# Optimization experiments

Measured on AMD Instinct MI355X. Metric: run time of the kernel, lower is better.

Reference implementation:

```python
import jax, jax.numpy as jnp
import numpy as np

KE = 14.3996454784255
P = 6  # polynomial cutoff order
A_EXP = 0.3
A_PREFACTOR = 0.4543
C = jnp.array([0.1818, 0.5099, 0.2802, 0.02817], dtype=jnp.float32)
K = jnp.array([3.2, 0.9423, 0.4028, 0.2016], dtype=jnp.float32)

N_NODES = 100000
N_EDGES = 6400000
N_ELEM = 10
N_RADII = 119


def setup_inputs() -> dict:
    key = jax.random.key(0)
    k1, k2, k3, k4, k5 = jax.random.split(key, 5)
    # edge distances in a physically plausible range (avoid x ~ 0 -> 1/x blowup)
    x = jax.random.uniform(k1, (N_EDGES, 1), dtype=jnp.float32) * 4.0 + 0.05
    node_attrs = jax.random.uniform(k2, (N_NODES, N_ELEM), dtype=jnp.float32)
    edge_index = jax.random.randint(k3, (2, N_EDGES), 0, N_NODES, dtype=jnp.int64)
    atomic_numbers = jax.random.randint(k4, (N_ELEM,), 1, N_RADII, dtype=jnp.int64)
    # covalent radii table (stand-in for ase.data.covalent_radii), ~0.3..2.6 Angstrom
    covalent_radii = 0.3 + 2.3 * jax.random.uniform(k5, (N_RADII,), dtype=jnp.float32)
    return {
        "x": x,
        "node_attrs": node_attrs,
        "edge_index": edge_index,
        "atomic_numbers": atomic_numbers,
        "covalent_radii": covalent_radii,
    }


def _envelope(x, r_max, p):
    r = x / r_max
    env = (1.0
           - (p + 1.0) * (p + 2.0) / 2.0 * r ** p
           + p * (p + 2.0) * r ** (p + 1)
           - p * (p + 1.0) / 2.0 * r ** (p + 2))
    return env * (x < r_max)


def reference(x, node_attrs, edge_index, atomic_numbers, covalent_radii):
    sender = edge_index[0]    # [E]
    receiver = edge_index[1]  # [E]
    # per-node atomic number from one-hot-ish node_attrs
    node_Z = atomic_numbers[jnp.argmax(node_attrs, axis=1)][:, None]  # [N,1] int
    Z_u = node_Z[sender]   # [E,1] int
    Z_v = node_Z[receiver] # [E,1] int
    Zu_f = Z_u.astype(x.dtype)
    Zv_f = Z_v.astype(x.dtype)
    a = A_PREFACTOR * 0.529 / (Zu_f ** A_EXP + Zv_f ** A_EXP)  # [E,1]
    r_over_a = x / a
    phi = (C[0] * jnp.exp(-K[0] * r_over_a)
           + C[1] * jnp.exp(-K[1] * r_over_a)
           + C[2] * jnp.exp(-K[2] * r_over_a)
           + C[3] * jnp.exp(-K[3] * r_over_a))
    v_edges = KE * Zu_f * Zv_f / x * phi  # [E,1]
    r_max = covalent_radii[Z_u[:, 0]][:, None] + covalent_radii[Z_v[:, 0]][:, None]  # [E,1]
    env = _envelope(x, r_max, float(P))
    v_edges = 0.5 * v_edges * env
    V_ZBL = jax.ops.segment_sum(v_edges, receiver, num_segments=node_attrs.shape[0])  # [N,1]
    return V_ZBL[:, 0]
```

## Files before the change

kernel.cpp:

```cpp
#include <hip/hip_runtime.h>

#define KE_CONST 14.3996454784255f

#define P2_SHIFT 15
#define P2_CHUNK 32768
#define SCAN_B2  64
#define SCAN_THR 1024
#define MAXC     4
#define MAXE     16

__global__ void zbl_prep_elem(const float* __restrict__ node_attrs,
                              unsigned char* __restrict__ elem,
                              int n_nodes, int n_elem) {
    int n = blockIdx.x * blockDim.x + threadIdx.x;
    if (n >= n_nodes) return;
    const float* row = node_attrs + (size_t)n * n_elem;
    float best = row[0];
    int bi = 0;
    for (int i = 1; i < n_elem; ++i) {
        float v = row[i];
        if (v > best) { best = v; bi = i; }
    }
    elem[n] = (unsigned char)bi;
}

__global__ void zbl_prep_pairs(const int* __restrict__ atomic_numbers,
                               const float* __restrict__ covalent_radii,
                               float4* __restrict__ pair_tab,
                               int n_elem) {
    int t = threadIdx.x;
    int np = n_elem * n_elem;
    if (t >= np) return;
    int eu = t / n_elem;
    int ev = t - eu * n_elem;
    int Zu = atomic_numbers[eu];
    int Zv = atomic_numbers[ev];
    float zu = (float)Zu, zv = (float)Zv;
    float inv_a = (__powf(zu, 0.3f) + __powf(zv, 0.3f)) * (1.0f / (0.4543f * 0.529f));
    float kezz  = 0.5f * KE_CONST * zu * zv;
    float rmax  = covalent_radii[Zu] + covalent_radii[Zv];
    pair_tab[t] = make_float4(inv_a, kezz, rmax, 1.0f / rmax);
}

__device__ __forceinline__ unsigned enc_val_p(float xv, const float4& pt) {
    float t = xv * pt.x;
    float phi = 0.1818f  * __expf(-3.2f    * t)
              + 0.5099f  * __expf(-0.9423f * t)
              + 0.2802f  * __expf(-0.4028f * t)
              + 0.02817f * __expf(-0.2016f * t);
    float rr = xv * pt.w;
    float r2 = rr * rr;
    float r6 = r2 * r2 * r2;
    float env = 1.0f - 28.0f * r6 + 48.0f * r6 * rr - 21.0f * r6 * r2;
    float val = fmaxf(pt.y * phi / xv * env, 0.0f);
    unsigned e = (__float_as_uint(val) + 0x8000u) >> 16;
    if (e > 0x7FFFu) e = 0x7FFFu;
    return (xv < pt.z) ? e : 0u;
}

__global__ __launch_bounds__(256)
void zbl_dense(const float* __restrict__ x,
               const int* __restrict__ ei,
               const unsigned char* __restrict__ elem,
               const float4* __restrict__ pair_tab,
               unsigned* __restrict__ packed,
               int n_edges, int n_elem) {
    __shared__ float4 pt[MAXE * MAXE];
    int np = n_elem * n_elem;
    for (int i = threadIdx.x; i < np; i += 256) pt[i] = pair_tab[i];
    __syncthreads();

    int t = blockIdx.x * blockDim.x + threadIdx.x;
    int base = t * 4;
    if (base + 4 <= n_edges) {
        int4   s4 = *(const int4*)(ei + base);
        int4   r4 = *(const int4*)(ei + n_edges + base);
        float4 x4 = *(const float4*)(x + base);
        unsigned es0 = elem[s4.x], es1 = elem[s4.y], es2 = elem[s4.z], es3 = elem[s4.w];
        unsigned er0 = elem[r4.x], er1 = elem[r4.y], er2 = elem[r4.z], er3 = elem[r4.w];
        float4 p0 = pt[es0 * n_elem + er0];
        float4 p1 = pt[es1 * n_elem + er1];
        float4 p2 = pt[es2 * n_elem + er2];
        float4 p3 = pt[es3 * n_elem + er3];
        uint4 o;
        o.x = ((unsigned)r4.x << 15) | enc_val_p(x4.x, p0);
        o.y = ((unsigned)r4.y << 15) | enc_val_p(x4.y, p1);
        o.z = ((unsigned)r4.z << 15) | enc_val_p(x4.z, p2);
        o.w = ((unsigned)r4.w << 15) | enc_val_p(x4.w, p3);
        *(uint4*)(packed + base) = o;
    } else {
        for (int e = base; e < n_edges; ++e) {
            unsigned es = elem[ei[e]];
            unsigned er = elem[ei[n_edges + e]];
            int r = ei[n_edges + e];
            packed[e] = ((unsigned)r << 15) | enc_val_p(x[e], pt[es * n_elem + er]);
        }
    }
}

__global__ __launch_bounds__(SCAN_THR)
void zbl_scan(const unsigned* __restrict__ packed,
              float* __restrict__ partial,
              int n_edges) {
    unsigned c = blockIdx.x >> 6;
    int      j = blockIdx.x & (SCAN_B2 - 1);

    __shared__ __align__(16) float acc[P2_CHUNK];
    for (int i = threadIdx.x * 4; i < P2_CHUNK; i += SCAN_THR * 4)
        *(float4*)&acc[i] = make_float4(0.f, 0.f, 0.f, 0.f);
    __syncthreads();

    long long e0 = (((long long)j * n_edges) / SCAN_B2) & ~3LL;
    long long e1 = (j == SCAN_B2 - 1) ? (long long)n_edges
                                      : ((((long long)(j + 1) * n_edges) / SCAN_B2) & ~3LL);
    long long vend = e1 & ~3LL;

    for (long long b = e0 + (long long)threadIdx.x * 4; b + 4 <= vend;
         b += (long long)SCAN_THR * 4) {
        uint4 p = *(const uint4*)(packed + b);
        if ((p.x >> 30) == c) atomicAdd(&acc[(p.x >> 15) & (P2_CHUNK - 1)],
                                        __uint_as_float((p.x & 0x7FFFu) << 16));
        if ((p.y >> 30) == c) atomicAdd(&acc[(p.y >> 15) & (P2_CHUNK - 1)],
                                        __uint_as_float((p.y & 0x7FFFu) << 16));
        if ((p.z >> 30) == c) atomicAdd(&acc[(p.z >> 15) & (P2_CHUNK - 1)],
                                        __uint_as_float((p.z & 0x7FFFu) << 16));
        if ((p.w >> 30) == c) atomicAdd(&acc[(p.w >> 15) & (P2_CHUNK - 1)],
                                        __uint_as_float((p.w & 0x7FFFu) << 16));
    }
    for (long long e = vend + threadIdx.x; e < e1; e += SCAN_THR) {
        unsigned w = packed[e];
        if ((w >> 30) == c) atomicAdd(&acc[(w >> 15) & (P2_CHUNK - 1)],
                                      __uint_as_float((w & 0x7FFFu) << 16));
    }

    __syncthreads();
    float* pp = partial + (size_t)blockIdx.x * P2_CHUNK;
    for (int i = threadIdx.x * 4; i < P2_CHUNK; i += SCAN_THR * 4)
        *(float4*)(pp + i) = *(const float4*)&acc[i];
}

__global__ void zbl_reduce(const float* __restrict__ partial,
                           float* __restrict__ out,
                           int n_nodes) {
    int i = blockIdx.x * blockDim.x + threadIdx.x;
    if (i >= n_nodes) return;
    int c  = i >> P2_SHIFT;
    int li = i & (P2_CHUNK - 1);
    const float* p = partial + ((size_t)c * SCAN_B2) * P2_CHUNK + li;
    float s0 = 0.f, s1 = 0.f, s2 = 0.f, s3 = 0.f;
    #pragma unroll
    for (int j = 0; j < SCAN_B2; j += 4) {
        s0 += p[(size_t)(j + 0) * P2_CHUNK];
        s1 += p[(size_t)(j + 1) * P2_CHUNK];
        s2 += p[(size_t)(j + 2) * P2_CHUNK];
        s3 += p[(size_t)(j + 3) * P2_CHUNK];
    }
    out[i] = (s0 + s1) + (s2 + s3);
}

__global__ void zbl_node_prep(const float* __restrict__ node_attrs,
                              const int* __restrict__ atomic_numbers,
                              const float* __restrict__ covalent_radii,
                              float4* __restrict__ node_data,
                              float* __restrict__ out_zero,
                              int n_nodes, int n_elem) {
    int n = blockIdx.x * blockDim.x + threadIdx.x;
    if (n >= n_nodes) return;
    const float* row = node_attrs + (size_t)n * n_elem;
    float best = row[0];
    int bi = 0;
    for (int i = 1; i < n_elem; ++i) {
        float v = row[i];
        if (v > best) { best = v; bi = i; }
    }
    int Z = atomic_numbers[bi];
    float zf = (float)Z;
    node_data[n] = make_float4(zf, __powf(zf, 0.3f), covalent_radii[Z], 0.0f);
    out_zero[n] = 0.0f;
}

__global__ void zbl_edge_atomic(const float* __restrict__ x,
                                const int* __restrict__ edge_index,
                                const float4* __restrict__ node_data,
                                float* __restrict__ out,
                                int n_edges) {
    int e = blockIdx.x * blockDim.x + threadIdx.x;
    if (e >= n_edges) return;
    int snd = edge_index[e];
    int r = edge_index[n_edges + e];
    float xv = x[e];
    float4 du = node_data[snd];
    float4 dv = node_data[r];
    float rmax = du.z + dv.z;
    if (xv >= rmax) return;
    const float inv_a_pref = 1.0f / (0.4543f * 0.529f);
    float t = xv * (du.y + dv.y) * inv_a_pref;
    float phi = 0.1818f  * __expf(-3.2f    * t)
              + 0.5099f  * __expf(-0.9423f * t)
              + 0.2802f  * __expf(-0.4028f * t)
              + 0.02817f * __expf(-0.2016f * t);
    float v = KE_CONST * du.x * dv.x * phi / xv;
    float rr = xv / rmax;
    float r2 = rr * rr;
    float r6 = r2 * r2 * r2;
    float env = 1.0f - 28.0f * r6 + 48.0f * r6 * rr - 21.0f * r6 * r2;
    atomicAdd(&out[r], 0.5f * v * env);
}

extern "C" void kernel_launch(void* const* d_in, const int* in_sizes, int n_in,
                              void* d_out, int out_size, void* d_ws, size_t ws_size,
                              hipStream_t stream) {
    const float* x              = (const float*)d_in[0];
    const float* node_attrs     = (const float*)d_in[1];
    const int*   edge_index     = (const int*)d_in[2];
    const int*   atomic_numbers = (const int*)d_in[3];
    const float* covalent_radii = (const float*)d_in[4];
    float* out = (float*)d_out;

    int n_edges = in_sizes[0];
    int n_elem  = in_sizes[3];
    int n_nodes = in_sizes[1] / n_elem;

    int C = (n_nodes + P2_CHUNK - 1) >> P2_SHIFT;
    size_t elem_bytes   = (((size_t)n_nodes) + 255) & ~(size_t)255;
    size_t pair_bytes   = ((size_t)MAXE * MAXE * sizeof(float4) + 255) & ~(size_t)255;
    size_t packed_bytes = (((size_t)n_edges * sizeof(unsigned)) + 255) & ~(size_t)255;
    size_t part_bytes   = (size_t)C * SCAN_B2 * P2_CHUNK * sizeof(float);
    bool fast = (C >= 1) && (C <= MAXC) && (n_nodes <= (1 << 17)) &&
                (n_elem >= 1) && (n_elem <= MAXE) && ((n_edges & 3) == 0) &&
                (ws_size >= elem_bytes + pair_bytes + packed_bytes + part_bytes);

    if (fast) {
        unsigned char* elem     = (unsigned char*)d_ws;
        float4*        pair_tab = (float4*)((char*)d_ws + elem_bytes);
        unsigned*      packed   = (unsigned*)((char*)d_ws + elem_bytes + pair_bytes);
        float*         part     = (float*)((char*)d_ws + elem_bytes + pair_bytes + packed_bytes);

        zbl_prep_elem<<<(n_nodes + 255) / 256, 256, 0, stream>>>(
            node_attrs, elem, n_nodes, n_elem);
        zbl_prep_pairs<<<1, 256, 0, stream>>>(
            atomic_numbers, covalent_radii, pair_tab, n_elem);

        zbl_dense<<<(n_edges / 4 + 255) / 256, 256, 0, stream>>>(
            x, edge_index, elem, pair_tab, packed, n_edges, n_elem);

        zbl_scan<<<C * SCAN_B2, SCAN_THR, 0, stream>>>(packed, part, n_edges);

        zbl_reduce<<<(n_nodes + 255) / 256, 256, 0, stream>>>(part, out, n_nodes);
        return;
    }

    float4* node_data = (float4*)d_ws;
    zbl_node_prep<<<(n_nodes + 255) / 256, 256, 0, stream>>>(
        node_attrs, atomic_numbers, covalent_radii, node_data,
        out, n_nodes, n_elem);
    zbl_edge_atomic<<<(n_edges + 255) / 256, 256, 0, stream>>>(
        x, edge_index, node_data, out, n_edges);
}
```

Before: 202.5 us.

## Fuse edge evaluation into chunked shared-memory scatter, dropping packed buffer

The separate dense pass that wrote packed receiver/bf16-value words is removed. Each scatter block now reads x, sender and receiver directly, computes the ZBL edge value in full fp32 and atomically adds it into its LDS chunk. This avoids writing and re-reading a 25.6 MB intermediate and one kernel launch. In exchange, every edge is recomputed once per node chunk (4 chunks), and the raw edge_index and x loads are read by each chunk instead of once.

```diff
diff --git a/kernel.cpp b/kernel.cpp
--- a/kernel.cpp
+++ b/kernel.cpp
@@ -42,95 +42,73 @@
     pair_tab[t] = make_float4(inv_a, kezz, rmax, 1.0f / rmax);
 }
 
-__device__ __forceinline__ unsigned enc_val_p(float xv, const float4& pt) {
-    float t = xv * pt.x;
+__device__ __forceinline__ float edge_val(float xv, const float4& p) {
+    float t = xv * p.x;
     float phi = 0.1818f  * __expf(-3.2f    * t)
               + 0.5099f  * __expf(-0.9423f * t)
               + 0.2802f  * __expf(-0.4028f * t)
               + 0.02817f * __expf(-0.2016f * t);
-    float rr = xv * pt.w;
+    float rr = xv * p.w;
     float r2 = rr * rr;
     float r6 = r2 * r2 * r2;
     float env = 1.0f - 28.0f * r6 + 48.0f * r6 * rr - 21.0f * r6 * r2;
-    float val = fmaxf(pt.y * phi / xv * env, 0.0f);
-    unsigned e = (__float_as_uint(val) + 0x8000u) >> 16;
-    if (e > 0x7FFFu) e = 0x7FFFu;
-    return (xv < pt.z) ? e : 0u;
-}
-
-__global__ __launch_bounds__(256)
-void zbl_dense(const float* __restrict__ x,
+    return p.y * phi / xv * env;
+}
+
+__global__ __launch_bounds__(SCAN_THR)
+void zbl_fused(const float* __restrict__ x,
                const int* __restrict__ ei,
                const unsigned char* __restrict__ elem,
                const float4* __restrict__ pair_tab,
-               unsigned* __restrict__ packed,
+               float* __restrict__ partial,
                int n_edges, int n_elem) {
+    unsigned c = blockIdx.x >> 6;
+    int      j = blockIdx.x & (SCAN_B2 - 1);
+
+    __shared__ __align__(16) float acc[P2_CHUNK];
     __shared__ float4 pt[MAXE * MAXE];
     int np = n_elem * n_elem;
-    for (int i = threadIdx.x; i < np; i += 256) pt[i] = pair_tab[i];
+    for (int i = threadIdx.x; i < np; i += SCAN_THR) pt[i] = pair_tab[i];
+    for (int i = threadIdx.x * 4; i < P2_CHUNK; i += SCAN_THR * 4)
+        *(float4*)&acc[i] = make_float4(0.f, 0.f, 0.f, 0.f);
     __syncthreads();
 
-    int t = blockIdx.x * blockDim.x + threadIdx.x;
-    int base = t * 4;
-    if (base + 4 <= n_edges) {
-        int4   s4 = *(const int4*)(ei + base);
-        int4   r4 = *(const int4*)(ei + n_edges + base);
-        float4 x4 = *(const float4*)(x + base);
+    const int* __restrict__ rcv = ei + n_edges;
+    long long e0 = (((long long)j * n_edges) / SCAN_B2) & ~3LL;
+    long long e1 = (j == SCAN_B2 - 1) ? (long long)n_edges
+                                      : ((((long long)(j + 1) * n_edges) / SCAN_B2) & ~3LL);
+    long long vend = e1 & ~3LL;
+
+    for (long long b = e0 + (long long)threadIdx.x * 4; b + 4 <= vend;
+         b += (long long)SCAN_THR * 4) {
+        int4   r4 = *(const int4*)(rcv + b);
+        int4   s4 = *(const int4*)(ei + b);
+        float4 x4 = *(const float4*)(x + b);
         unsigned es0 = elem[s4.x], es1 = elem[s4.y], es2 = elem[s4.z], es3 = elem[s4.w];
         unsigned er0 = elem[r4.x], er1 = elem[r4.y], er2 = elem[r4.z], er3 = elem[r4.w];
         float4 p0 = pt[es0 * n_elem + er0];
         float4 p1 = pt[es1 * n_elem + er1];
         float4 p2 = pt[es2 * n_elem + er2];
         float4 p3 = pt[es3 * n_elem + er3];
-        uint4 o;
-        o.x = ((unsigned)r4.x << 15) | enc_val_p(x4.x, p0);
-        o.y = ((unsigned)r4.y << 15) | enc_val_p(x4.y, p1);
-        o.z = ((unsigned)r4.z << 15) | enc_val_p(x4.z, p2);
-        o.w = ((unsigned)r4.w << 15) | enc_val_p(x4.w, p3);
-        *(uint4*)(packed + base) = o;
-    } else {
-        for (int e = base; e < n_edges; ++e) {
-            unsigned es = elem[ei[e]];
-            unsigned er = elem[ei[n_edges + e]];
-            int r = ei[n_edges + e];
-            packed[e] = ((unsigned)r << 15) | enc_val_p(x[e], pt[es * n_elem + er]);
-        }
-    }
-}
-
-__global__ __launch_bounds__(SCAN_THR)
-void zbl_scan(const unsigned* __restrict__ packed,
-              float* __restrict__ partial,
-              int n_edges) {
-    unsigned c = blockIdx.x >> 6;
-    int      j = blockIdx.x & (SCAN_B2 - 1);
-
-    __shared__ __align__(16) float acc[P2_CHUNK];
-    for (int i = threadIdx.x * 4; i < P2_CHUNK; i += SCAN_THR * 4)
-        *(float4*)&acc[i] = make_float4(0.f, 0.f, 0.f, 0.f);
-    __syncthreads();
-
-    long long e0 = (((long long)j * n_edges) / SCAN_B2) & ~3LL;
-    long long e1 = (j == SCAN_B2 - 1) ? (long long)n_edges
-                                      : ((((long long)(j + 1) * n_edges) / SCAN_B2) & ~3LL);
-    long long vend = e1 & ~3LL;
-
-    for (long long b = e0 + (long long)threadIdx.x * 4; b + 4 <= vend;
-         b += (long long)SCAN_THR * 4) {
-        uint4 p = *(const uint4*)(packed + b);
-        if ((p.x >> 30) == c) atomicAdd(&acc[(p.x >> 15) & (P2_CHUNK - 1)],
-                                        __uint_as_float((p.x & 0x7FFFu) << 16));
-        if ((p.y >> 30) == c) atomicAdd(&acc[(p.y >> 15) & (P2_CHUNK - 1)],
-                                        __uint_as_float((p.y & 0x7FFFu) << 16));
-        if ((p.z >> 30) == c) atomicAdd(&acc[(p.z >> 15) & (P2_CHUNK - 1)],
-                                        __uint_as_float((p.z & 0x7FFFu) << 16));
-        if ((p.w >> 30) == c) atomicAdd(&acc[(p.w >> 15) & (P2_CHUNK - 1)],
-                                        __uint_as_float((p.w & 0x7FFFu) << 16));
+        float v0 = edge_val(x4.x, p0);
+        float v1 = edge_val(x4.y, p1);
+        float v2 = edge_val(x4.z, p2);
+        float v3 = edge_val(x4.w, p3);
+        if (((unsigned)(r4.x >> P2_SHIFT) == c) & (x4.x < p0.z))
+            atomicAdd(&acc[r4.x & (P2_CHUNK - 1)], v0);
+        if (((unsigned)(r4.y >> P2_SHIFT) == c) & (x4.y < p1.z))
+            atomicAdd(&acc[r4.y & (P2_CHUNK - 1)], v1);
+        if (((unsigned)(r4.z >> P2_SHIFT) == c) & (x4.z < p2.z))
+            atomicAdd(&acc[r4.z & (P2_CHUNK - 1)], v2);
+        if (((unsigned)(r4.w >> P2_SHIFT) == c) & (x4.w < p3.z))
+            atomicAdd(&acc[r4.w & (P2_CHUNK - 1)], v3);
     }
     for (long long e = vend + threadIdx.x; e < e1; e += SCAN_THR) {
-        unsigned w = packed[e];
-        if ((w >> 30) == c) atomicAdd(&acc[(w >> 15) & (P2_CHUNK - 1)],
-                                      __uint_as_float((w & 0x7FFFu) << 16));
+        int r = rcv[e];
+        if ((unsigned)(r >> P2_SHIFT) != c) continue;
+        float4 p = pt[elem[ei[e]] * n_elem + elem[r]];
+        float xv = x[e];
+        if (xv < p.z) atomicAdd(&acc[r & (P2_CHUNK - 1)], edge_val(xv, p));
     }
 
     __syncthreads();
@@ -222,29 +200,25 @@
     int n_nodes = in_sizes[1] / n_elem;
 
     int C = (n_nodes + P2_CHUNK - 1) >> P2_SHIFT;
-    size_t elem_bytes   = (((size_t)n_nodes) + 255) & ~(size_t)255;
-    size_t pair_bytes   = ((size_t)MAXE * MAXE * sizeof(float4) + 255) & ~(size_t)255;
-    size_t packed_bytes = (((size_t)n_edges * sizeof(unsigned)) + 255) & ~(size_t)255;
-    size_t part_bytes   = (size_t)C * SCAN_B2 * P2_CHUNK * sizeof(float);
+    size_t elem_bytes = (((size_t)n_nodes) + 255) & ~(size_t)255;
+    size_t pair_bytes = ((size_t)MAXE * MAXE * sizeof(float4) + 255) & ~(size_t)255;
+    size_t part_bytes = (size_t)C * SCAN_B2 * P2_CHUNK * sizeof(float);
     bool fast = (C >= 1) && (C <= MAXC) && (n_nodes <= (1 << 17)) &&
-                (n_elem >= 1) && (n_elem <= MAXE) && ((n_edges & 3) == 0) &&
-                (ws_size >= elem_bytes + pair_bytes + packed_bytes + part_bytes);
+                (n_elem >= 1) && (n_elem <= MAXE) &&
+                (ws_size >= elem_bytes + pair_bytes + part_bytes);
 
     if (fast) {
         unsigned char* elem     = (unsigned char*)d_ws;
         float4*        pair_tab = (float4*)((char*)d_ws + elem_bytes);
-        unsigned*      packed   = (unsigned*)((char*)d_ws + elem_bytes + pair_bytes);
-        float*         part     = (float*)((char*)d_ws + elem_bytes + pair_bytes + packed_bytes);
+        float*         part     = (float*)((char*)d_ws + elem_bytes + pair_bytes);
 
         zbl_prep_elem<<<(n_nodes + 255) / 256, 256, 0, stream>>>(
             node_attrs, elem, n_nodes, n_elem);
         zbl_prep_pairs<<<1, 256, 0, stream>>>(
             atomic_numbers, covalent_radii, pair_tab, n_elem);
 
-        zbl_dense<<<(n_edges / 4 + 255) / 256, 256, 0, stream>>>(
-            x, edge_index, elem, pair_tab, packed, n_edges, n_elem);
-
-        zbl_scan<<<C * SCAN_B2, SCAN_THR, 0, stream>>>(packed, part, n_edges);
+        zbl_fused<<<C * SCAN_B2, SCAN_THR, 0, stream>>>(
+            x, edge_index, elem, pair_tab, part, n_edges, n_elem);
 
         zbl_reduce<<<(n_nodes + 255) / 256, 256, 0, stream>>>(part, out, n_nodes);
         return;
```

Result: slower. 268.3 us (+32.5%).

## Stage node element table in LDS for dense edge pass with persistent blocks

Applied to the files above, without the earlier changes.

The dense edge kernel now copies the whole per-node element byte table (up to 128 KB) into shared memory in each block. The per-edge sender and receiver element lookups then hit LDS instead of issuing random global byte gathers. To pay for that copy, the kernel switches to 256 persistent blocks of 1024 threads, each striding over a contiguous edge range, with a scalar tail loop that also drops the old requirement that the edge count be a multiple of four. The cost is repeated table loads per block and only one block per CU because of the large LDS footprint.

```diff
diff --git a/kernel.cpp b/kernel.cpp
--- a/kernel.cpp
+++ b/kernel.cpp
@@ -8,6 +8,9 @@
 #define SCAN_THR 1024
 #define MAXC     4
 #define MAXE     16
+#define ELEM_CAP 131072
+#define DN_THR   1024
+#define DN_BLOCKS 256
 
 __global__ void zbl_prep_elem(const float* __restrict__ node_attrs,
                               unsigned char* __restrict__ elem,
@@ -42,40 +45,51 @@
     pair_tab[t] = make_float4(inv_a, kezz, rmax, 1.0f / rmax);
 }
 
-__device__ __forceinline__ unsigned enc_val_p(float xv, const float4& pt) {
-    float t = xv * pt.x;
+__device__ __forceinline__ unsigned enc_val_p(float xv, const float4& p) {
+    float t = xv * p.x;
     float phi = 0.1818f  * __expf(-3.2f    * t)
               + 0.5099f  * __expf(-0.9423f * t)
               + 0.2802f  * __expf(-0.4028f * t)
               + 0.02817f * __expf(-0.2016f * t);
-    float rr = xv * pt.w;
+    float rr = xv * p.w;
     float r2 = rr * rr;
     float r6 = r2 * r2 * r2;
     float env = 1.0f - 28.0f * r6 + 48.0f * r6 * rr - 21.0f * r6 * r2;
-    float val = fmaxf(pt.y * phi / xv * env, 0.0f);
+    float val = fmaxf(p.y * phi / xv * env, 0.0f);
     unsigned e = (__float_as_uint(val) + 0x8000u) >> 16;
     if (e > 0x7FFFu) e = 0x7FFFu;
-    return (xv < pt.z) ? e : 0u;
-}
-
-__global__ __launch_bounds__(256)
-void zbl_dense(const float* __restrict__ x,
-               const int* __restrict__ ei,
-               const unsigned char* __restrict__ elem,
-               const float4* __restrict__ pair_tab,
-               unsigned* __restrict__ packed,
-               int n_edges, int n_elem) {
+    return (xv < p.z) ? e : 0u;
+}
+
+__global__ __launch_bounds__(DN_THR)
+void zbl_dense_lds(const float* __restrict__ x,
+                   const int* __restrict__ ei,
+                   const unsigned char* __restrict__ elem_g,
+                   const float4* __restrict__ pair_tab,
+                   unsigned* __restrict__ packed,
+                   int n_edges, int n_elem, int n_nodes) {
+    __shared__ __align__(16) unsigned char elem[ELEM_CAP];
     __shared__ float4 pt[MAXE * MAXE];
+
     int np = n_elem * n_elem;
-    for (int i = threadIdx.x; i < np; i += 256) pt[i] = pair_tab[i];
+    for (int i = threadIdx.x; i < np; i += DN_THR) pt[i] = pair_tab[i];
+    int nwords = (n_nodes + 15) >> 4;
+    const uint4* eg4 = (const uint4*)elem_g;
+    uint4* el4 = (uint4*)elem;
+    for (int i = threadIdx.x; i < nwords; i += DN_THR) el4[i] = eg4[i];
     __syncthreads();
 
-    int t = blockIdx.x * blockDim.x + threadIdx.x;
-    int base = t * 4;
-    if (base + 4 <= n_edges) {
-        int4   s4 = *(const int4*)(ei + base);
-        int4   r4 = *(const int4*)(ei + n_edges + base);
-        float4 x4 = *(const float4*)(x + base);
+    long long e0 = (((long long)blockIdx.x * n_edges) / DN_BLOCKS) & ~3LL;
+    long long e1 = (blockIdx.x == DN_BLOCKS - 1)
+                     ? (long long)n_edges
+                     : ((((long long)(blockIdx.x + 1) * n_edges) / DN_BLOCKS) & ~3LL);
+    long long vend = e1 & ~3LL;
+
+    for (long long b = e0 + (long long)threadIdx.x * 4; b + 4 <= vend;
+         b += (long long)DN_THR * 4) {
+        int4   s4 = *(const int4*)(ei + b);
+        int4   r4 = *(const int4*)(ei + n_edges + b);
+        float4 x4 = *(const float4*)(x + b);
         unsigned es0 = elem[s4.x], es1 = elem[s4.y], es2 = elem[s4.z], es3 = elem[s4.w];
         unsigned er0 = elem[r4.x], er1 = elem[r4.y], er2 = elem[r4.z], er3 = elem[r4.w];
         float4 p0 = pt[es0 * n_elem + er0];
@@ -87,14 +101,12 @@
         o.y = ((unsigned)r4.y << 15) | enc_val_p(x4.y, p1);
         o.z = ((unsigned)r4.z << 15) | enc_val_p(x4.z, p2);
         o.w = ((unsigned)r4.w << 15) | enc_val_p(x4.w, p3);
-        *(uint4*)(packed + base) = o;
-    } else {
-        for (int e = base; e < n_edges; ++e) {
-            unsigned es = elem[ei[e]];
-            unsigned er = elem[ei[n_edges + e]];
-            int r = ei[n_edges + e];
-            packed[e] = ((unsigned)r << 15) | enc_val_p(x[e], pt[es * n_elem + er]);
-        }
+        *(uint4*)(packed + b) = o;
+    }
+    for (long long e = vend + threadIdx.x; e < e1; e += DN_THR) {
+        int r = ei[n_edges + e];
+        float4 p = pt[elem[ei[e]] * n_elem + elem[r]];
+        packed[e] = ((unsigned)r << 15) | enc_val_p(x[e], p);
     }
 }
 
@@ -226,8 +238,8 @@
     size_t pair_bytes   = ((size_t)MAXE * MAXE * sizeof(float4) + 255) & ~(size_t)255;
     size_t packed_bytes = (((size_t)n_edges * sizeof(unsigned)) + 255) & ~(size_t)255;
     size_t part_bytes   = (size_t)C * SCAN_B2 * P2_CHUNK * sizeof(float);
-    bool fast = (C >= 1) && (C <= MAXC) && (n_nodes <= (1 << 17)) &&
-                (n_elem >= 1) && (n_elem <= MAXE) && ((n_edges & 3) == 0) &&
+    bool fast = (C >= 1) && (C <= MAXC) && (n_nodes <= ELEM_CAP) &&
+                (n_elem >= 1) && (n_elem <= MAXE) &&
                 (ws_size >= elem_bytes + pair_bytes + packed_bytes + part_bytes);
 
     if (fast) {
@@ -241,8 +253,8 @@
         zbl_prep_pairs<<<1, 256, 0, stream>>>(
             atomic_numbers, covalent_radii, pair_tab, n_elem);
 
-        zbl_dense<<<(n_edges / 4 + 255) / 256, 256, 0, stream>>>(
-            x, edge_index, elem, pair_tab, packed, n_edges, n_elem);
+        zbl_dense_lds<<<DN_BLOCKS, DN_THR, 0, stream>>>(
+            x, edge_index, elem, pair_tab, packed, n_edges, n_elem, n_nodes);
 
         zbl_scan<<<C * SCAN_B2, SCAN_THR, 0, stream>>>(packed, part, n_edges);
 
```

New measurement: 168.6 us. 16.7% less time.
